# Kernel optimization log

Hardware: AMD Instinct MI355X
Metric: run time of the kernel (lower is better)

Reference implementation:

```python
import jax, jax.numpy as jnp
import numpy as np

B, N, H, E = 1, 50000, 8, 32
P = 1_600_000  # num edges


def setup_inputs() -> dict:
    key = jax.random.key(0)
    kq, kk, kv, ka = jax.random.split(key, 4)
    queries = jax.random.normal(kq, (B, N, H, E), dtype=jnp.float32)
    keys = jax.random.normal(kk, (B, N, H, E), dtype=jnp.float32)
    values = jax.random.normal(kv, (B, N, H, E), dtype=jnp.float32)
    adj = jax.random.randint(ka, (2, P), 0, N, dtype=jnp.int32)
    return {"queries": queries, "keys": keys, "values": values, "adj": adj}


def reference(queries, keys, values, adj):
    # queries/keys: (B, N, H, E); values: (B, N, H, D); adj: (2, P) COO edges
    b, n, h, e = queries.shape
    temp = 1.0 / np.sqrt(e).astype(np.float32)
    src, dst = adj[0], adj[1]
    # per-edge scaled dot product: (P, B, H), edge axis leading for segment ops
    s = temp * jnp.einsum("bphe,bphe->pbh", queries[:, src], keys[:, dst])
    # segment (scatter) softmax keyed by target node src
    m = jax.ops.segment_max(s, src, num_segments=n)          # (N, B, H)
    p = jnp.exp(s - m[src])                                   # (P, B, H)
    den = jax.ops.segment_sum(p, src, num_segments=n)        # (N, B, H)
    alpha = p / den[src]                                      # (P, B, H)
    # sparse weighted aggregation (spmm): out[i] = sum_{e: src==i} alpha_e * v[dst_e]
    vg = jnp.moveaxis(values[:, dst], 0, 1)                   # (P, B, H, D)
    out = jax.ops.segment_sum(alpha[..., None] * vg, src, num_segments=n)  # (N, B, H, D)
    return jnp.moveaxis(out, 0, 1)                            # (B, N, H, D)
```

## Files before the change

kernel.cpp:

```cpp
#include <hip/hip_runtime.h>
#include <hip/hip_fp16.h>
#include <math.h>

#define HEADS 8
#define EDIM 32
#define ROW (HEADS * EDIM)

__device__ __forceinline__ void pack_one(const float* __restrict__ k, const float* __restrict__ v,
                                         uint4* __restrict__ kvh, long t) {
    const float4 kf = *reinterpret_cast<const float4*>(k + t * 4);
    const float4 vf = *reinterpret_cast<const float4*>(v + t * 4);
    __half2 h0 = __floats2half2_rn(kf.x, kf.y);
    __half2 h1 = __floats2half2_rn(kf.z, kf.w);
    __half2 h2 = __floats2half2_rn(vf.x, vf.y);
    __half2 h3 = __floats2half2_rn(vf.z, vf.w);
    uint4 o;
    o.x = *reinterpret_cast<unsigned int*>(&h0);
    o.y = *reinterpret_cast<unsigned int*>(&h1);
    o.z = *reinterpret_cast<unsigned int*>(&h2);
    o.w = *reinterpret_cast<unsigned int*>(&h3);
    kvh[t] = o;
}

__global__ __launch_bounds__(256) void prep_fused_kernel(
    const float* __restrict__ k, const float* __restrict__ v, uint4* __restrict__ kvh,
    const int* __restrict__ src, const int* __restrict__ dst,
    int* __restrict__ counts, int* __restrict__ padded,
    int N, int P, int packBlocks, int cap, int copies)
{
    if ((int)blockIdx.x < packBlocks) {
        const long t = (long)blockIdx.x * 256 + threadIdx.x;
        if (t < (long)N * 64) pack_one(k, v, kvh, t);
    } else {
        const int copy = (int)blockIdx.x & (copies - 1);
        int* __restrict__ cnt = counts + (size_t)copy * N;
        int* __restrict__ pad = padded + (size_t)copy * N * cap;
        int i = ((int)blockIdx.x - packBlocks) * 256 + threadIdx.x;
        const int stride = ((int)gridDim.x - packBlocks) * 256;
        for (; i < P; i += stride) {
            const int s = src[i];
            const int pos = atomicAdd(&cnt[s], 1);
            if (pos < cap) pad[(size_t)s * cap + pos] = dst[i];
        }
    }
}

__global__ __launch_bounds__(256) void pack_kernel(const float* __restrict__ k,
                                                   const float* __restrict__ v,
                                                   uint4* __restrict__ kvh, long total) {
    const long t = (long)blockIdx.x * blockDim.x + threadIdx.x;
    if (t < total) pack_one(k, v, kvh, t);
}

__global__ void hist_kernel(const int* __restrict__ src, int* __restrict__ counts, int P) {
    int i = blockIdx.x * blockDim.x + threadIdx.x;
    int stride = gridDim.x * blockDim.x;
    for (; i < P; i += stride) atomicAdd(&counts[src[i]], 1);
}

__global__ __launch_bounds__(1024) void scan_block(const int* __restrict__ counts,
                                                   int* __restrict__ loc_excl,
                                                   int* __restrict__ bsums, int n) {
    __shared__ int wsum[16];
    const int lane = threadIdx.x & 63;
    const int wv = threadIdx.x >> 6;
    const int i = blockIdx.x * 1024 + threadIdx.x;
    const int val = (i < n) ? counts[i] : 0;
    int incl = val;
    #pragma unroll
    for (int off = 1; off < 64; off <<= 1) {
        int t = __shfl_up(incl, off);
        if (lane >= off) incl += t;
    }
    if (lane == 63) wsum[wv] = incl;
    __syncthreads();
    if (threadIdx.x < 16) {
        int wval = wsum[threadIdx.x];
        int winc = wval;
        #pragma unroll
        for (int off = 1; off < 16; off <<= 1) {
            int t = __shfl_up(winc, off);
            if ((int)threadIdx.x >= off) winc += t;
        }
        wsum[threadIdx.x] = winc - wval;
    }
    __syncthreads();
    const int ex = wsum[wv] + incl - val;
    if (i < n) loc_excl[i] = ex;
    if (threadIdx.x == 1023) bsums[blockIdx.x] = ex + val;
}

__global__ void scan_tops(const int* __restrict__ bsums, int* __restrict__ bbase,
                          int nb, int* __restrict__ total_out) {
    const int lane = threadIdx.x & 63;
    int base = 0;
    for (int start = 0; start < nb; start += 64) {
        const int idx = start + lane;
        const int v = (idx < nb) ? bsums[idx] : 0;
        int incl = v;
        #pragma unroll
        for (int off = 1; off < 64; off <<= 1) {
            int t = __shfl_up(incl, off);
            if (lane >= off) incl += t;
        }
        if (idx < nb) bbase[idx] = base + incl - v;
        base += __shfl(incl, 63);
    }
    if (lane == 0) *total_out = base;
}

__global__ void scan_add(const int* __restrict__ loc_excl, const int* __restrict__ bbase,
                         int* __restrict__ offsets, int* __restrict__ cursors, int n) {
    const int i = blockIdx.x * blockDim.x + threadIdx.x;
    if (i < n) {
        const int o = loc_excl[i] + bbase[i >> 10];
        offsets[i] = o;
        cursors[i] = o;
    }
}

__global__ void scatter_kernel(const int* __restrict__ src, const int* __restrict__ dst,
                               int* __restrict__ cursors, int* __restrict__ sorted_dst, int P) {
    int i = blockIdx.x * blockDim.x + threadIdx.x;
    int stride = gridDim.x * blockDim.x;
    for (; i < P; i += stride) {
        int s = src[i];
        int pos = atomicAdd(&cursors[s], 1);
        sorted_dst[pos] = dst[i];
    }
}

__device__ __forceinline__ void edge_accum(const uint4 raw, const float4 qv,
                                           float& lsum, float4& acc) {
    const float2 k01 = __half22float2(*reinterpret_cast<const __half2*>(&raw.x));
    const float2 k23 = __half22float2(*reinterpret_cast<const __half2*>(&raw.y));
    const float2 v01 = __half22float2(*reinterpret_cast<const __half2*>(&raw.z));
    const float2 v23 = __half22float2(*reinterpret_cast<const __half2*>(&raw.w));
    float p = qv.x * k01.x + qv.y * k01.y + qv.z * k23.x + qv.w * k23.y;
    p += __shfl_xor(p, 1);
    p += __shfl_xor(p, 2);
    p += __shfl_xor(p, 4);
    const float w = __expf(p);
    lsum += w;
    acc.x += w * v01.x; acc.y += w * v01.y;
    acc.z += w * v23.x; acc.w += w * v23.y;
}

__global__ __launch_bounds__(256) void attn_kernel_h(
    const float* __restrict__ q, const uint4* __restrict__ kv,
    const int* __restrict__ counts_or_offsets, const int* __restrict__ edges,
    float* __restrict__ out, int N, float temp, int cap, int copies)
{
    const int wave = threadIdx.x >> 6;
    const int lane = threadIdx.x & 63;
    const int node = blockIdx.x * 4 + wave;
    if (node >= N) return;

    float4 qv = *reinterpret_cast<const float4*>(q + (size_t)node * ROW + lane * 4);
    qv.x *= temp; qv.y *= temp; qv.z *= temp; qv.w *= temp;
    const uint4* kvl = kv + lane;

    float lsum = 0.0f;
    float4 acc = {0.f, 0.f, 0.f, 0.f};

    if (cap > 0) {
        for (int c = 0; c < copies; ++c) {
            int cnt = counts_or_offsets[(size_t)c * N + node];
            cnt = (cnt < cap) ? cnt : cap;
            const int* __restrict__ bucket = edges + ((size_t)c * N + node) * cap;
            int i = 0;
            for (; i + 2 <= cnt; i += 2) {
                const int d0 = bucket[i];
                const int d1 = bucket[i + 1];
                const uint4 r0 = kvl[(size_t)d0 * 64];
                const uint4 r1 = kvl[(size_t)d1 * 64];
                edge_accum(r0, qv, lsum, acc);
                edge_accum(r1, qv, lsum, acc);
            }
            if (i < cnt) {
                const uint4 r = kvl[(size_t)bucket[i] * 64];
                edge_accum(r, qv, lsum, acc);
            }
        }
    } else {
        int e = counts_or_offsets[node];
        const int end = counts_or_offsets[node + 1];
        for (; e + 2 <= end; e += 2) {
            const int d0 = edges[e];
            const int d1 = edges[e + 1];
            const uint4 r0 = kvl[(size_t)d0 * 64];
            const uint4 r1 = kvl[(size_t)d1 * 64];
            edge_accum(r0, qv, lsum, acc);
            edge_accum(r1, qv, lsum, acc);
        }
        if (e < end) {
            const uint4 r = kvl[(size_t)edges[e] * 64];
            edge_accum(r, qv, lsum, acc);
        }
    }

    const float inv = (lsum > 0.0f) ? (1.0f / lsum) : 0.0f;
    float4 o;
    o.x = acc.x * inv; o.y = acc.y * inv; o.z = acc.z * inv; o.w = acc.w * inv;
    *reinterpret_cast<float4*>(out + (size_t)node * ROW + lane * 4) = o;
}

extern "C" void kernel_launch(void* const* d_in, const int* in_sizes, int n_in,
                              void* d_out, int out_size, void* d_ws, size_t ws_size,
                              hipStream_t stream) {
    const float* q = (const float*)d_in[0];
    const float* k = (const float*)d_in[1];
    const float* v = (const float*)d_in[2];
    const int*   adj = (const int*)d_in[3];

    const int N = in_sizes[0] / ROW;
    const int P = in_sizes[3] / 2;
    const int* src = adj;
    const int* dst = adj + P;

    const float temp = 1.0f / sqrtf((float)EDIM);
    const size_t kv_bytes = (size_t)N * 64 * sizeof(uint4);

    const int tier_copies[3] = {8, 4, 1};
    const int tier_cap[3]    = {20, 28, 96};

    for (int t = 0; t < 3; ++t) {
        const int copies = tier_copies[t];
        const int cap = tier_cap[t];
        const size_t int_bytes = (size_t)copies * N * (1 + cap) * sizeof(int);
        const size_t kv_off = (int_bytes + 15) & ~(size_t)15;
        if (ws_size < kv_off + kv_bytes) continue;

        int* counts = (int*)d_ws;
        int* padded = counts + (size_t)copies * N;
        uint4* kvh = (uint4*)((char*)d_ws + kv_off);

        hipMemsetAsync(counts, 0, (size_t)copies * N * sizeof(int), stream);

        const int packBlocks = (int)(((long)N * 64 + 255) / 256);
        const int scatBlocks = 2048;
        prep_fused_kernel<<<packBlocks + scatBlocks, 256, 0, stream>>>(
            k, v, kvh, src, dst, counts, padded, N, P, packBlocks, cap, copies);

        attn_kernel_h<<<(N + 3) / 4, 256, 0, stream>>>(q, kvh, counts, padded,
                                                       (float*)d_out, N, temp, cap, copies);
        return;
    }

    const int nb = (N + 1023) / 1024;
    int* counts  = (int*)d_ws;
    int* offsets = counts + N;
    int* cursors = offsets + N + 1;
    int* sorted  = cursors + N;
    int* bsums   = sorted + P;
    int* bbase   = bsums + nb;
    size_t int_bytes = (size_t)(3 * N + 1 + P + 2 * nb) * sizeof(int);
    size_t kv_off = (int_bytes + 15) & ~(size_t)15;
    uint4* kvh = (uint4*)((char*)d_ws + kv_off);

    hipMemsetAsync(counts, 0, (size_t)N * sizeof(int), stream);
    pack_kernel<<<(int)(((long)N * 64 + 255) / 256), 256, 0, stream>>>(k, v, kvh, (long)N * 64);
    hist_kernel<<<2048, 256, 0, stream>>>(src, counts, P);
    scan_block<<<nb, 1024, 0, stream>>>(counts, counts, bsums, N);
    scan_tops<<<1, 64, 0, stream>>>(bsums, bbase, nb, offsets + N);
    scan_add<<<(N + 255) / 256, 256, 0, stream>>>(counts, bbase, offsets, cursors, N);
    scatter_kernel<<<2048, 256, 0, stream>>>(src, dst, cursors, sorted, P);
    attn_kernel_h<<<(N + 3) / 4, 256, 0, stream>>>(q, kvh, offsets, sorted,
                                                   (float*)d_out, N, temp, 0, 1);
}
```

Measured before the change: 341.6 us.

## Use fp16 dot2 for scores, vectorize edge scatter, reorder prep blocks

The attention kernel now converts the scaled query to packed fp16 and computes each per-lane partial score with v_dot2 fp16 instructions instead of converting keys to fp32 and doing scalar FMAs. The fused prep kernel puts the scatter blocks first, raises their count to 3072, and loads src/dst as int2 pairs so each thread handles two edges per iteration. The aim is fewer ALU ops in the hot loop and better overlap of the atomic-heavy scatter with the pack work. Rounding the query to fp16 reduces score precision.

```diff
diff --git a/kernel.cpp b/kernel.cpp
--- a/kernel.cpp
+++ b/kernel.cpp
@@ -5,6 +5,8 @@
 #define HEADS 8
 #define EDIM 32
 #define ROW (HEADS * EDIM)
+
+typedef _Float16 h2_t __attribute__((ext_vector_type(2)));
 
 __device__ __forceinline__ void pack_one(const float* __restrict__ k, const float* __restrict__ v,
                                          uint4* __restrict__ kvh, long t) {
@@ -26,22 +28,31 @@
     const float* __restrict__ k, const float* __restrict__ v, uint4* __restrict__ kvh,
     const int* __restrict__ src, const int* __restrict__ dst,
     int* __restrict__ counts, int* __restrict__ padded,
-    int N, int P, int packBlocks, int cap, int copies)
+    int N, int P, int scatBlocks, int cap, int copies)
 {
-    if ((int)blockIdx.x < packBlocks) {
-        const long t = (long)blockIdx.x * 256 + threadIdx.x;
-        if (t < (long)N * 64) pack_one(k, v, kvh, t);
-    } else {
+    if ((int)blockIdx.x < scatBlocks) {
         const int copy = (int)blockIdx.x & (copies - 1);
         int* __restrict__ cnt = counts + (size_t)copy * N;
         int* __restrict__ pad = padded + (size_t)copy * N * cap;
-        int i = ((int)blockIdx.x - packBlocks) * 256 + threadIdx.x;
-        const int stride = ((int)gridDim.x - packBlocks) * 256;
-        for (; i < P; i += stride) {
-            const int s = src[i];
+        const int P2 = P >> 1;
+        const int stride = scatBlocks * 256;
+        int i = (int)blockIdx.x * 256 + threadIdx.x;
+        for (; i < P2; i += stride) {
+            const int2 s2 = reinterpret_cast<const int2*>(src)[i];
+            const int2 d2 = reinterpret_cast<const int2*>(dst)[i];
+            int pos = atomicAdd(&cnt[s2.x], 1);
+            if (pos < cap) pad[(size_t)s2.x * cap + pos] = d2.x;
+            pos = atomicAdd(&cnt[s2.y], 1);
+            if (pos < cap) pad[(size_t)s2.y * cap + pos] = d2.y;
+        }
+        if ((P & 1) && blockIdx.x == 0 && threadIdx.x == 0) {
+            const int s = src[P - 1];
             const int pos = atomicAdd(&cnt[s], 1);
-            if (pos < cap) pad[(size_t)s * cap + pos] = dst[i];
-        }
+            if (pos < cap) pad[(size_t)s * cap + pos] = dst[P - 1];
+        }
+    } else {
+        const long t = (long)((int)blockIdx.x - scatBlocks) * 256 + threadIdx.x;
+        if (t < (long)N * 64) pack_one(k, v, kvh, t);
     }
 }
 
@@ -130,13 +141,14 @@
     }
 }
 
-__device__ __forceinline__ void edge_accum(const uint4 raw, const float4 qv,
+__device__ __forceinline__ void edge_accum(const uint4 raw, const h2_t qh01, const h2_t qh23,
                                            float& lsum, float4& acc) {
-    const float2 k01 = __half22float2(*reinterpret_cast<const __half2*>(&raw.x));
-    const float2 k23 = __half22float2(*reinterpret_cast<const __half2*>(&raw.y));
+    const h2_t k01 = *reinterpret_cast<const h2_t*>(&raw.x);
+    const h2_t k23 = *reinterpret_cast<const h2_t*>(&raw.y);
     const float2 v01 = __half22float2(*reinterpret_cast<const __half2*>(&raw.z));
     const float2 v23 = __half22float2(*reinterpret_cast<const __half2*>(&raw.w));
-    float p = qv.x * k01.x + qv.y * k01.y + qv.z * k23.x + qv.w * k23.y;
+    float p = __builtin_amdgcn_fdot2(qh01, k01,
+              __builtin_amdgcn_fdot2(qh23, k23, 0.0f, false), false);
     p += __shfl_xor(p, 1);
     p += __shfl_xor(p, 2);
     p += __shfl_xor(p, 4);
@@ -158,6 +170,10 @@
 
     float4 qv = *reinterpret_cast<const float4*>(q + (size_t)node * ROW + lane * 4);
     qv.x *= temp; qv.y *= temp; qv.z *= temp; qv.w *= temp;
+    const __half2 qp01 = __floats2half2_rn(qv.x, qv.y);
+    const __half2 qp23 = __floats2half2_rn(qv.z, qv.w);
+    const h2_t qh01 = *reinterpret_cast<const h2_t*>(&qp01);
+    const h2_t qh23 = *reinterpret_cast<const h2_t*>(&qp23);
     const uint4* kvl = kv + lane;
 
     float lsum = 0.0f;
@@ -174,12 +190,12 @@
                 const int d1 = bucket[i + 1];
                 const uint4 r0 = kvl[(size_t)d0 * 64];
                 const uint4 r1 = kvl[(size_t)d1 * 64];
-                edge_accum(r0, qv, lsum, acc);
-                edge_accum(r1, qv, lsum, acc);
+                edge_accum(r0, qh01, qh23, lsum, acc);
+                edge_accum(r1, qh01, qh23, lsum, acc);
             }
             if (i < cnt) {
                 const uint4 r = kvl[(size_t)bucket[i] * 64];
-                edge_accum(r, qv, lsum, acc);
+                edge_accum(r, qh01, qh23, lsum, acc);
             }
         }
     } else {
@@ -190,12 +206,12 @@
             const int d1 = edges[e + 1];
             const uint4 r0 = kvl[(size_t)d0 * 64];
             const uint4 r1 = kvl[(size_t)d1 * 64];
-            edge_accum(r0, qv, lsum, acc);
-            edge_accum(r1, qv, lsum, acc);
+            edge_accum(r0, qh01, qh23, lsum, acc);
+            edge_accum(r1, qh01, qh23, lsum, acc);
         }
         if (e < end) {
             const uint4 r = kvl[(size_t)edges[e] * 64];
-            edge_accum(r, qv, lsum, acc);
+            edge_accum(r, qh01, qh23, lsum, acc);
         }
     }
 
@@ -238,9 +254,9 @@
         hipMemsetAsync(counts, 0, (size_t)copies * N * sizeof(int), stream);
 
         const int packBlocks = (int)(((long)N * 64 + 255) / 256);
-        const int scatBlocks = 2048;
-        prep_fused_kernel<<<packBlocks + scatBlocks, 256, 0, stream>>>(
-            k, v, kvh, src, dst, counts, padded, N, P, packBlocks, cap, copies);
+        const int scatBlocks = 3072;
+        prep_fused_kernel<<<scatBlocks + packBlocks, 256, 0, stream>>>(
+            k, v, kvh, src, dst, counts, padded, N, P, scatBlocks, cap, copies);
 
         attn_kernel_h<<<(N + 3) / 4, 256, 0, stream>>>(q, kvh, counts, padded,
                                                        (float*)d_out, N, temp, cap, copies);
```

Result: slower. 378.3 us (+10.7%).
